# Kernel optimization log

Hardware: AMD Instinct MI355X
Metric: run time of the kernel (lower is better)

The kernel has to match this reference:

```python
import jax, jax.numpy as jnp
from jax import lax
import numpy as np

B, S, D, COMP = 4, 1024, 512, 4


def setup_inputs() -> dict:
    key = jax.random.key(0)
    x = jax.random.normal(key, (B * S, D), dtype=jnp.float32)
    return {"x": x, "comp_rate": COMP, "seqlen": S}


def _merge_step(x, t, seq):
    # x: [seq, D], compacted so the k = seq - t valid tokens occupy rows 0..k-1.
    xn = jnp.roll(x, -1, axis=0)  # x[i+1] (wrap value never selected among valid pairs)
    # dist only feeds argmax (non-differentiable), mirror torch exactly; stop_gradient
    # keeps the vjp from saving residuals for this dead-for-gradients path.
    xg = lax.stop_gradient(x)
    dist = jnp.sum(xg * jnp.roll(xg, -1, axis=0), axis=-1)  # scalar_product metric
    j = jnp.arange(x.shape[0])
    dist = jnp.where(j < seq - 1 - t, dist, -jnp.inf)  # k-1 valid adjacent pairs
    mid = jnp.argmax(dist)
    jm = j[:, None]
    # rows < mid keep, row mid becomes (x[mid]+x[mid+1])/2, rows > mid shift left by 1
    return jnp.where(jm < mid, x, jnp.where(jm == mid, (x + xn) * 0.5, xn))


def _merge_sample(x, steps, seq):
    def body(carry, t):
        return _merge_step(carry, t, seq), None
    x, _ = lax.scan(body, x, jnp.arange(steps))
    return x


def reference(x, comp_rate, seqlen):
    d = x.shape[-1]
    b = x.shape[0] // seqlen
    n_comp = seqlen // comp_rate
    steps = seqlen - n_comp
    xb = x.reshape(b, seqlen, d)
    merged = jax.vmap(lambda xs: _merge_sample(xs, steps, seqlen))(xb)
    # torch smart_merge concatenates per-sample results along dim 0
    return merged[:, :n_comp].reshape(b * n_comp, d)
```

## Files before the change

### kernel.cpp

```cpp
#include <hip/hip_runtime.h>
#include <math.h>

#define S 1024
#define D 512
#define NCOMP (S / 4)
#define STEPS (S - NCOMP)
#define NW 16
#define NEG_INF (-__builtin_inff())

__device__ __forceinline__ int   f2i(float x) { return __builtin_bit_cast(int, x); }
__device__ __forceinline__ float i2f(int x)   { return __builtin_bit_cast(float, x); }

__device__ __forceinline__ unsigned fkey(float f) {
    unsigned u = __builtin_bit_cast(unsigned, f);
    return (u & 0x80000000u) ? ~u : (u | 0x80000000u);
}

__device__ __forceinline__ float wave_sum63(float x) {
    x += i2f(__builtin_amdgcn_update_dpp(0, f2i(x), 0x111, 0xF, 0xF, true));
    x += i2f(__builtin_amdgcn_update_dpp(0, f2i(x), 0x112, 0xF, 0xF, true));
    x += i2f(__builtin_amdgcn_update_dpp(0, f2i(x), 0x114, 0xF, 0xF, true));
    x += i2f(__builtin_amdgcn_update_dpp(0, f2i(x), 0x118, 0xF, 0xF, true));
    x += i2f(__builtin_amdgcn_update_dpp(0, f2i(x), 0x142, 0xA, 0xF, true));
    x += i2f(__builtin_amdgcn_update_dpp(0, f2i(x), 0x143, 0xC, 0xF, true));
    return x;
}

#define AMAX_STEP(ctrl, rm) do {                                                        \
    unsigned ok_ = (unsigned)__builtin_amdgcn_update_dpp((int)key, (int)key, (ctrl), (rm), 0xF, false); \
    int      oi_ = __builtin_amdgcn_update_dpp(bi, bi, (ctrl), (rm), 0xF, false);        \
    bool tk_ = (ok_ > key) || ((ok_ == key) && (oi_ < bi));                              \
    key = tk_ ? ok_ : key; bi = tk_ ? oi_ : bi;                                          \
} while (0)

__device__ __forceinline__ float dot8_partial(float4 a0, float4 a1, float4 b0, float4 b1) {
    float acc = a0.x * b0.x;
    acc += a0.y * b0.y; acc += a0.z * b0.z; acc += a0.w * b0.w;
    acc += a1.x * b1.x; acc += a1.y * b1.y; acc += a1.z * b1.z; acc += a1.w * b1.w;
    return acc;
}

__device__ __forceinline__ void dist_set(float (&dv)[16], bool ln, int k, float val) {
    switch (k) {
        case 0:  if (ln) dv[0]  = val; break;
        case 1:  if (ln) dv[1]  = val; break;
        case 2:  if (ln) dv[2]  = val; break;
        case 3:  if (ln) dv[3]  = val; break;
        case 4:  if (ln) dv[4]  = val; break;
        case 5:  if (ln) dv[5]  = val; break;
        case 6:  if (ln) dv[6]  = val; break;
        case 7:  if (ln) dv[7]  = val; break;
        case 8:  if (ln) dv[8]  = val; break;
        case 9:  if (ln) dv[9]  = val; break;
        case 10: if (ln) dv[10] = val; break;
        case 11: if (ln) dv[11] = val; break;
        case 12: if (ln) dv[12] = val; break;
        case 13: if (ln) dv[13] = val; break;
        case 14: if (ln) dv[14] = val; break;
        case 15: if (ln) dv[15] = val; break;
    }
}

__global__ __launch_bounds__(1024) void pool_merge_kernel(
    const float* __restrict__ x, float* __restrict__ out, float* vals_base) {
    const int b    = blockIdx.x;
    const int tid  = threadIdx.x;
    const int lane = tid & 63;
    const int wave = tid >> 6;

    float* vals = vals_base + (size_t)b * S * D;
    const float* xin = x + (size_t)b * S * D;

    __shared__ int4  links[S];
    __shared__ float sdist[S];
    __shared__ int   outIdx[NCOMP];

    if (vals != (float*)xin) {
        const float4* s4 = (const float4*)xin;
        float4* d4 = (float4*)vals;
        for (int i = tid; i < S * D / 4; i += 1024) d4[i] = s4[i];
    }
    for (int s = tid; s < S; s += 1024)
        links[s] = make_int4(s - 1, s + 1, (s + 2 <= S) ? s + 2 : S, 0);
    __syncthreads();

    for (int pr = wave; pr < S - 1; pr += NW) {
        const float4* a4 = (const float4*)(vals + (size_t)pr * D);
        const float4* b4 = (const float4*)(vals + (size_t)(pr + 1) * D);
        float4 a0 = a4[lane * 2], a1 = a4[lane * 2 + 1];
        float4 b0 = b4[lane * 2], b1 = b4[lane * 2 + 1];
        float tot = wave_sum63(dot8_partial(a0, a1, b0, b1));
        if (lane == 63) sdist[pr] = tot;
    }
    if (tid == 0) sdist[S - 1] = NEG_INF;
    __syncthreads();

    if (wave == 0) {
        float dv[16];
#pragma unroll
        for (int k = 0; k < 16; ++k) dv[k] = sdist[lane + 64 * k];

        for (int t = 0; t < STEPS; ++t) {
            float v8[8]; int k8[8];
#pragma unroll
            for (int k = 0; k < 8; ++k) { bool tk = dv[k+8] > dv[k]; v8[k] = tk ? dv[k+8] : dv[k]; k8[k] = tk ? (k+8) : k; }
            float v4[4]; int k4[4];
#pragma unroll
            for (int k = 0; k < 4; ++k) { bool tk = v8[k+4] > v8[k]; v4[k] = tk ? v8[k+4] : v8[k]; k4[k] = tk ? k8[k+4] : k8[k]; }
            float v2[2]; int k2[2];
#pragma unroll
            for (int k = 0; k < 2; ++k) { bool tk = v4[k+2] > v4[k]; v2[k] = tk ? v4[k+2] : v4[k]; k2[k] = tk ? k4[k+2] : k4[k]; }
            bool tk1 = v2[1] > v2[0];
            float lv = tk1 ? v2[1] : v2[0];
            int   lk = tk1 ? k2[1] : k2[0];

            unsigned key = fkey(lv);
            int bi = lane | (lk << 6);
            AMAX_STEP(0x111, 0xF); AMAX_STEP(0x112, 0xF);
            AMAX_STEP(0x114, 0xF); AMAX_STEP(0x118, 0xF);
            AMAX_STEP(0x142, 0xA); AMAX_STEP(0x143, 0xC);
            const int m = __builtin_amdgcn_readlane(bi, 63);

            int4 L = links[m];
            const int p = __builtin_amdgcn_readfirstlane(L.x);
            const int r = __builtin_amdgcn_readfirstlane(L.y);
            const int q = __builtin_amdgcn_readfirstlane(L.z);
            const bool hasp = (p >= 0), hasq = (q < S);

            const float4* pm = (const float4*)(vals + (size_t)m * D);
            const float4* pr4 = (const float4*)(vals + (size_t)r * D);
            float4 am0 = pm[lane * 2],  am1 = pm[lane * 2 + 1];
            float4 ar0 = pr4[lane * 2], ar1 = pr4[lane * 2 + 1];
            float4 ap0, ap1, aq0, aq1;
            if (hasp) { const float4* pp = (const float4*)(vals + (size_t)p * D); ap0 = pp[lane * 2]; ap1 = pp[lane * 2 + 1]; }
            if (hasq) { const float4* pq = (const float4*)(vals + (size_t)q * D); aq0 = pq[lane * 2]; aq1 = pq[lane * 2 + 1]; }

            int n2r = __builtin_amdgcn_readfirstlane(links[r].z);

            float4 vm0, vm1;
            vm0.x = (am0.x + ar0.x) * 0.5f; vm0.y = (am0.y + ar0.y) * 0.5f;
            vm0.z = (am0.z + ar0.z) * 0.5f; vm0.w = (am0.w + ar0.w) * 0.5f;
            vm1.x = (am1.x + ar1.x) * 0.5f; vm1.y = (am1.y + ar1.y) * 0.5f;
            vm1.z = (am1.z + ar1.z) * 0.5f; vm1.w = (am1.w + ar1.w) * 0.5f;
            ((float4*)(vals + (size_t)m * D))[lane * 2]     = vm0;
            ((float4*)(vals + (size_t)m * D))[lane * 2 + 1] = vm1;

            if (lane == 0) {
                links[m].y = q;
                links[m].z = n2r;
                if (hasp) links[p].z = q;
                if (hasq) links[q].x = m;
            }

            float ndm = NEG_INF, ndp = 0.0f;
            if (hasq) {
                float s_ = wave_sum63(dot8_partial(vm0, vm1, aq0, aq1));
                ndm = i2f(__builtin_amdgcn_readlane(f2i(s_), 63));
            }
            if (hasp) {
                float s_ = wave_sum63(dot8_partial(ap0, ap1, vm0, vm1));
                ndp = i2f(__builtin_amdgcn_readlane(f2i(s_), 63));
            }
            dist_set(dv, lane == (r & 63), r >> 6, NEG_INF);
            dist_set(dv, lane == (m & 63), m >> 6, ndm);
            if (hasp) dist_set(dv, lane == (p & 63), p >> 6, ndp);
        }
    }
    __syncthreads();

    if (tid == 0) {
        int s = 0;
        for (int i = 0; i < NCOMP; ++i) { outIdx[i] = s; s = links[s].y; }
    }
    __syncthreads();

    float* outb = out + (size_t)b * NCOMP * D;
    for (int i = wave; i < NCOMP; i += NW) {
        const float4* sr = (const float4*)(vals + (size_t)outIdx[i] * D);
        float4* dr = (float4*)(outb + (size_t)i * D);
        dr[lane * 2]     = sr[lane * 2];
        dr[lane * 2 + 1] = sr[lane * 2 + 1];
    }
}

extern "C" void kernel_launch(void* const* d_in, const int* in_sizes, int n_in,
                              void* d_out, int out_size, void* d_ws, size_t ws_size,
                              hipStream_t stream) {
    const float* x = (const float*)d_in[0];
    float* out = (float*)d_out;
    const int b = in_sizes[0] / (S * D);
    const size_t need = (size_t)in_sizes[0] * sizeof(float);
    float* vals = (ws_size >= need) ? (float*)d_ws : (float*)x;
    pool_merge_kernel<<<dim3(b), dim3(1024), 0, stream>>>(x, out, vals);
}
```

Before: 1.100 ms.

## Split merge into init/merge/gather kernels with speculative prefetch of next-step rows

Splits the single kernel into three launches. A wide init kernel copies the input and computes the initial adjacent-pair dot products across 16 blocks per sample, a single-wave serial merge kernel runs the loop, and a multi-block gather kernel copies out the kept rows. Inside the merge loop the argmax reads distances from LDS. The rows and links needed for the next step are loaded speculatively for both neighbour-merge cases and for the global-max case, so global-memory latency overlaps the argmax reduction. Intermediate distances and output indices are staged in the output buffer. The trade-offs are extra launches, more complex carry logic and more registers.

Result: faster. 1.052 ms (-4.4%).

```diff
diff --git a/kernel.cpp b/kernel.cpp
--- a/kernel.cpp
+++ b/kernel.cpp
@@ -5,7 +5,6 @@
 #define D 512
 #define NCOMP (S / 4)
 #define STEPS (S - NCOMP)
-#define NW 16
 #define NEG_INF (-__builtin_inff())
 
 __device__ __forceinline__ int   f2i(float x) { return __builtin_bit_cast(int, x); }
@@ -14,6 +13,10 @@
 __device__ __forceinline__ unsigned fkey(float f) {
     unsigned u = __builtin_bit_cast(unsigned, f);
     return (u & 0x80000000u) ? ~u : (u | 0x80000000u);
+}
+__device__ __forceinline__ float unfkey(unsigned k) {
+    unsigned u = (k & 0x80000000u) ? (k & 0x7fffffffu) : ~k;
+    return __builtin_bit_cast(float, u);
 }
 
 __device__ __forceinline__ float wave_sum63(float x) {
@@ -33,153 +36,214 @@
     key = tk_ ? ok_ : key; bi = tk_ ? oi_ : bi;                                          \
 } while (0)
 
-__device__ __forceinline__ float dot8_partial(float4 a0, float4 a1, float4 b0, float4 b1) {
-    float acc = a0.x * b0.x;
-    acc += a0.y * b0.y; acc += a0.z * b0.z; acc += a0.w * b0.w;
-    acc += a1.x * b1.x; acc += a1.y * b1.y; acc += a1.z * b1.z; acc += a1.w * b1.w;
+struct Row { float4 a, b; };
+
+__device__ __forceinline__ Row row_load(const float* vals, int slot, int lane) {
+    const float4* p = (const float4*)(vals + (size_t)slot * D);
+    Row r; r.a = p[lane * 2]; r.b = p[lane * 2 + 1]; return r;
+}
+__device__ __forceinline__ void row_store(float* vals, int slot, int lane, Row r) {
+    float4* p = (float4*)(vals + (size_t)slot * D);
+    p[lane * 2] = r.a; p[lane * 2 + 1] = r.b;
+}
+__device__ __forceinline__ Row row_avg(Row x, Row y) {
+    Row r;
+    r.a.x = (x.a.x + y.a.x) * 0.5f; r.a.y = (x.a.y + y.a.y) * 0.5f;
+    r.a.z = (x.a.z + y.a.z) * 0.5f; r.a.w = (x.a.w + y.a.w) * 0.5f;
+    r.b.x = (x.b.x + y.b.x) * 0.5f; r.b.y = (x.b.y + y.b.y) * 0.5f;
+    r.b.z = (x.b.z + y.b.z) * 0.5f; r.b.w = (x.b.w + y.b.w) * 0.5f;
+    return r;
+}
+__device__ __forceinline__ float dot8_partial(Row x, Row y) {
+    float acc = x.a.x * y.a.x;
+    acc += x.a.y * y.a.y; acc += x.a.z * y.a.z; acc += x.a.w * y.a.w;
+    acc += x.b.x * y.b.x; acc += x.b.y * y.b.y; acc += x.b.z * y.b.z; acc += x.b.w * y.b.w;
     return acc;
 }
-
-__device__ __forceinline__ void dist_set(float (&dv)[16], bool ln, int k, float val) {
-    switch (k) {
-        case 0:  if (ln) dv[0]  = val; break;
-        case 1:  if (ln) dv[1]  = val; break;
-        case 2:  if (ln) dv[2]  = val; break;
-        case 3:  if (ln) dv[3]  = val; break;
-        case 4:  if (ln) dv[4]  = val; break;
-        case 5:  if (ln) dv[5]  = val; break;
-        case 6:  if (ln) dv[6]  = val; break;
-        case 7:  if (ln) dv[7]  = val; break;
-        case 8:  if (ln) dv[8]  = val; break;
-        case 9:  if (ln) dv[9]  = val; break;
-        case 10: if (ln) dv[10] = val; break;
-        case 11: if (ln) dv[11] = val; break;
-        case 12: if (ln) dv[12] = val; break;
-        case 13: if (ln) dv[13] = val; break;
-        case 14: if (ln) dv[14] = val; break;
-        case 15: if (ln) dv[15] = val; break;
-    }
-}
-
-__global__ __launch_bounds__(1024) void pool_merge_kernel(
-    const float* __restrict__ x, float* __restrict__ out, float* vals_base) {
-    const int b    = blockIdx.x;
-    const int tid  = threadIdx.x;
-    const int lane = tid & 63;
-    const int wave = tid >> 6;
-
-    float* vals = vals_base + (size_t)b * S * D;
-    const float* xin = x + (size_t)b * S * D;
-
-    __shared__ int4  links[S];
-    __shared__ float sdist[S];
-    __shared__ int   outIdx[NCOMP];
-
-    if (vals != (float*)xin) {
-        const float4* s4 = (const float4*)xin;
-        float4* d4 = (float4*)vals;
-        for (int i = tid; i < S * D / 4; i += 1024) d4[i] = s4[i];
-    }
-    for (int s = tid; s < S; s += 1024)
-        links[s] = make_int4(s - 1, s + 1, (s + 2 <= S) ? s + 2 : S, 0);
+__device__ __forceinline__ int lsr(int s) { return ((unsigned)s < (unsigned)S) ? s : 0; }
+__device__ __forceinline__ int lsl(int s) { return ((unsigned)s <= (unsigned)S) ? s : 0; }
+
+__device__ __forceinline__ void lds_argmax(const float* dist, int lane, float& v1, int& i1) {
+    float av[16];
+#pragma unroll
+    for (int k = 0; k < 16; ++k) av[k] = dist[lane + 64 * k];
+    float v8[8]; int k8[8];
+#pragma unroll
+    for (int k = 0; k < 8; ++k) { bool tk = av[k+8] > av[k]; v8[k] = tk ? av[k+8] : av[k]; k8[k] = tk ? (k+8) : k; }
+    float v4[4]; int k4[4];
+#pragma unroll
+    for (int k = 0; k < 4; ++k) { bool tk = v8[k+4] > v8[k]; v4[k] = tk ? v8[k+4] : v8[k]; k4[k] = tk ? k8[k+4] : k8[k]; }
+    float v2[2]; int k2[2];
+#pragma unroll
+    for (int k = 0; k < 2; ++k) { bool tk = v4[k+2] > v4[k]; v2[k] = tk ? v4[k+2] : v4[k]; k2[k] = tk ? k4[k+2] : k4[k]; }
+    bool tk1 = v2[1] > v2[0];
+    float lv = tk1 ? v2[1] : v2[0];
+    int   lk = tk1 ? k2[1] : k2[0];
+    unsigned key = fkey(lv);
+    int bi = lane | (lk << 6);
+    AMAX_STEP(0x111, 0xF); AMAX_STEP(0x112, 0xF);
+    AMAX_STEP(0x114, 0xF); AMAX_STEP(0x118, 0xF);
+    AMAX_STEP(0x142, 0xA); AMAX_STEP(0x143, 0xC);
+    i1 = __builtin_amdgcn_readlane(bi, 63);
+    v1 = unfkey((unsigned)__builtin_amdgcn_readlane((int)key, 63));
+}
+
+__global__ __launch_bounds__(256) void init_kernel(const float* __restrict__ x,
+                                                   float* __restrict__ vals,
+                                                   float* __restrict__ out) {
+    const int blk = blockIdx.x, b = blk >> 4, g = blk & 15;
+    const int tid = threadIdx.x, lane = tid & 63, w = tid >> 6;
+    const float* xb = x + (size_t)b * S * D;
+    if (vals != x) {
+        float* vb = vals + (size_t)b * S * D;
+        const float4* s4 = (const float4*)xb;
+        float4* d4 = (float4*)vb;
+        const int base = g * (S * D / 4 / 16);
+        for (int i = tid; i < S * D / 4 / 16; i += 256) d4[base + i] = s4[base + i];
+    }
+    float* sd = out + (size_t)b * NCOMP * D;
+#pragma unroll 1
+    for (int j = 0; j < 16; ++j) {
+        int pr = g * 64 + w * 16 + j;
+        if (pr < S - 1) {
+            Row A = row_load(xb, pr, lane);
+            Row B = row_load(xb, pr + 1, lane);
+            float t = wave_sum63(dot8_partial(A, B));
+            if (lane == 63) sd[pr] = t;
+        }
+    }
+    if (g == 0 && tid == 0) sd[S - 1] = NEG_INF;
+}
+
+__global__ __launch_bounds__(64) void merge_kernel(float* __restrict__ vals,
+                                                   float* __restrict__ out) {
+    const int b = blockIdx.x, lane = threadIdx.x;
+    float* vb = vals + (size_t)b * S * D;
+    float* aux = out + (size_t)b * NCOMP * D;
+    const float* sd = aux;
+    int* outIdx = (int*)(aux + S);
+
+    __shared__ int4  links[S + 1];
+    __shared__ float dist[S];
+
+#pragma unroll
+    for (int k = 0; k < 16; ++k) {
+        int s = lane + 64 * k;
+        links[s] = make_int4(s - 1, s + 1, (s + 2 <= S) ? (s + 2) : S, 0);
+        dist[s] = sd[s];
+    }
+    if (lane == 0) links[S] = make_int4(S, S, S, 0);
+
+    float v1; int i1;
+    lds_argmax(dist, lane, v1, i1);
+    int m = i1;
+    int4 L0 = links[m];
+    int p = __builtin_amdgcn_readfirstlane(L0.x);
+    int r = __builtin_amdgcn_readfirstlane(L0.y);
+    int q = __builtin_amdgcn_readfirstlane(L0.z);
+    bool hasp = (p >= 0), hasq = (q < S);
+    int pp = hasp ? __builtin_amdgcn_readfirstlane(links[p].x) : -1;
+    int nq = hasq ? __builtin_amdgcn_readfirstlane(links[q].y) : S;
+    Row Rp  = row_load(vb, lsr(p),  lane);
+    Row Rm  = row_load(vb, m,       lane);
+    Row Rr  = row_load(vb, r,       lane);
+    Row Rq  = row_load(vb, lsr(q),  lane);
+    Row Rpp = row_load(vb, lsr(pp), lane);
+    Row Rnq = row_load(vb, lsr(nq), lane);
+
+#pragma unroll 1
+    for (int t = 0; t < STEPS; ++t) {
+        if (lane == 0) {
+            links[m].y = q; links[m].z = nq;
+            if (hasp) links[p].z = q;
+            if (hasq) links[q].x = m;
+            dist[m] = NEG_INF; dist[r] = NEG_INF;
+            if (hasp) dist[p] = NEG_INF;
+        }
+        Row vm = row_avg(Rm, Rr);
+        row_store(vb, m, lane, vm);
+        if (t + 1 >= STEPS) break;
+
+        float sp_ = wave_sum63(dot8_partial(Rp, vm));
+        float sq_ = wave_sum63(dot8_partial(vm, Rq));
+        float ndp = hasp ? i2f(__builtin_amdgcn_readlane(f2i(sp_), 63)) : NEG_INF;
+        float ndm = hasq ? i2f(__builtin_amdgcn_readlane(f2i(sq_), 63)) : NEG_INF;
+
+        lds_argmax(dist, lane, v1, i1);
+
+        float best = v1; int bi = i1;
+        if (hasp && (ndp > best || (ndp == best && p < bi))) { best = ndp; bi = p; }
+        if (hasq && (ndm > best || (ndm == best && m < bi))) { best = ndm; bi = m; }
+        const int m2 = bi;
+
+        if (lane == 0) {
+            if (hasp) dist[p] = ndp;
+            if (hasq) dist[m] = ndm;
+        }
+
+        int4 Li = links[lsl(i1)];
+        int p2 = __builtin_amdgcn_readfirstlane(Li.x);
+        int r2 = __builtin_amdgcn_readfirstlane(Li.y);
+        int q2 = __builtin_amdgcn_readfirstlane(Li.z);
+        int4 Lp2 = links[lsl(p2)];
+        int4 Lq2 = links[lsl(q2)];
+        int pp2 = (p2 >= 0) ? __builtin_amdgcn_readfirstlane(Lp2.x) : -1;
+        int nq2 = (q2 < S)  ? __builtin_amdgcn_readfirstlane(Lq2.y) : S;
+        Row Sp  = (p2 == m)  ? vm : row_load(vb, lsr(p2),  lane);
+        Row Si  = row_load(vb, lsr(i1), lane);
+        Row Sr  = row_load(vb, lsr(r2), lane);
+        Row Sq  = (q2 == m)  ? vm : row_load(vb, lsr(q2),  lane);
+        Row Spp = (pp2 == m) ? vm : row_load(vb, lsr(pp2), lane);
+        Row Snq = (nq2 == m) ? vm : row_load(vb, lsr(nq2), lane);
+
+        if (m2 == m) {
+            int nnq = S;
+            if (nq < S) nnq = __builtin_amdgcn_readfirstlane(links[nq].y);
+            Row Rnq2 = (nnq < S) ? row_load(vb, lsr(nnq), lane) : Rnq;
+            Rm = vm; Rr = Rq; Rq = Rnq; Rnq = Rnq2;
+            r = q; q = nq; nq = nnq;
+            hasq = (q < S);
+        } else if (m2 == p) {
+            int npp = -1;
+            if (pp >= 0) npp = __builtin_amdgcn_readfirstlane(links[pp].x);
+            Row Rpp2 = (npp >= 0) ? row_load(vb, lsr(npp), lane) : Rpp;
+            Rr = vm; Rm = Rp; Rp = Rpp; Rpp = Rpp2;
+            r = m; m = p; p = pp; pp = npp;
+            hasp = (p >= 0);
+        } else {
+            m = i1; p = p2; r = r2; q = q2; pp = pp2; nq = nq2;
+            Rm = Si; Rr = Sr; Rp = Sp; Rq = Sq; Rpp = Spp; Rnq = Snq;
+            hasp = (p >= 0); hasq = (q < S);
+        }
+    }
+
+    if (lane == 0) {
+        int s = 0;
+        for (int i = 0; i < NCOMP; i += 2) {
+            outIdx[i] = s;
+            int4 Ls = links[s];
+            if (i + 1 < NCOMP) outIdx[i + 1] = Ls.y;
+            s = Ls.z;
+        }
+    }
+}
+
+__global__ __launch_bounds__(256) void gather_kernel(const float* __restrict__ vals,
+                                                     float* __restrict__ out) {
+    const int b = blockIdx.x, part = blockIdx.y;
+    const float* vb = vals + (size_t)b * S * D;
+    float* ob = out + (size_t)b * NCOMP * D;
+    __shared__ int oi[NCOMP / 8];
+    const int row0 = part * (NCOMP / 8);
+    if (threadIdx.x < NCOMP / 8)
+        oi[threadIdx.x] = ((const int*)(ob + S))[row0 + threadIdx.x];
     __syncthreads();
-
-    for (int pr = wave; pr < S - 1; pr += NW) {
-        const float4* a4 = (const float4*)(vals + (size_t)pr * D);
-        const float4* b4 = (const float4*)(vals + (size_t)(pr + 1) * D);
-        float4 a0 = a4[lane * 2], a1 = a4[lane * 2 + 1];
-        float4 b0 = b4[lane * 2], b1 = b4[lane * 2 + 1];
-        float tot = wave_sum63(dot8_partial(a0, a1, b0, b1));
-        if (lane == 63) sdist[pr] = tot;
-    }
-    if (tid == 0) sdist[S - 1] = NEG_INF;
-    __syncthreads();
-
-    if (wave == 0) {
-        float dv[16];
-#pragma unroll
-        for (int k = 0; k < 16; ++k) dv[k] = sdist[lane + 64 * k];
-
-        for (int t = 0; t < STEPS; ++t) {
-            float v8[8]; int k8[8];
-#pragma unroll
-            for (int k = 0; k < 8; ++k) { bool tk = dv[k+8] > dv[k]; v8[k] = tk ? dv[k+8] : dv[k]; k8[k] = tk ? (k+8) : k; }
-            float v4[4]; int k4[4];
-#pragma unroll
-            for (int k = 0; k < 4; ++k) { bool tk = v8[k+4] > v8[k]; v4[k] = tk ? v8[k+4] : v8[k]; k4[k] = tk ? k8[k+4] : k8[k]; }
-            float v2[2]; int k2[2];
-#pragma unroll
-            for (int k = 0; k < 2; ++k) { bool tk = v4[k+2] > v4[k]; v2[k] = tk ? v4[k+2] : v4[k]; k2[k] = tk ? k4[k+2] : k4[k]; }
-            bool tk1 = v2[1] > v2[0];
-            float lv = tk1 ? v2[1] : v2[0];
-            int   lk = tk1 ? k2[1] : k2[0];
-
-            unsigned key = fkey(lv);
-            int bi = lane | (lk << 6);
-            AMAX_STEP(0x111, 0xF); AMAX_STEP(0x112, 0xF);
-            AMAX_STEP(0x114, 0xF); AMAX_STEP(0x118, 0xF);
-            AMAX_STEP(0x142, 0xA); AMAX_STEP(0x143, 0xC);
-            const int m = __builtin_amdgcn_readlane(bi, 63);
-
-            int4 L = links[m];
-            const int p = __builtin_amdgcn_readfirstlane(L.x);
-            const int r = __builtin_amdgcn_readfirstlane(L.y);
-            const int q = __builtin_amdgcn_readfirstlane(L.z);
-            const bool hasp = (p >= 0), hasq = (q < S);
-
-            const float4* pm = (const float4*)(vals + (size_t)m * D);
-            const float4* pr4 = (const float4*)(vals + (size_t)r * D);
-            float4 am0 = pm[lane * 2],  am1 = pm[lane * 2 + 1];
-            float4 ar0 = pr4[lane * 2], ar1 = pr4[lane * 2 + 1];
-            float4 ap0, ap1, aq0, aq1;
-            if (hasp) { const float4* pp = (const float4*)(vals + (size_t)p * D); ap0 = pp[lane * 2]; ap1 = pp[lane * 2 + 1]; }
-            if (hasq) { const float4* pq = (const float4*)(vals + (size_t)q * D); aq0 = pq[lane * 2]; aq1 = pq[lane * 2 + 1]; }
-
-            int n2r = __builtin_amdgcn_readfirstlane(links[r].z);
-
-            float4 vm0, vm1;
-            vm0.x = (am0.x + ar0.x) * 0.5f; vm0.y = (am0.y + ar0.y) * 0.5f;
-            vm0.z = (am0.z + ar0.z) * 0.5f; vm0.w = (am0.w + ar0.w) * 0.5f;
-            vm1.x = (am1.x + ar1.x) * 0.5f; vm1.y = (am1.y + ar1.y) * 0.5f;
-            vm1.z = (am1.z + ar1.z) * 0.5f; vm1.w = (am1.w + ar1.w) * 0.5f;
-            ((float4*)(vals + (size_t)m * D))[lane * 2]     = vm0;
-            ((float4*)(vals + (size_t)m * D))[lane * 2 + 1] = vm1;
-
-            if (lane == 0) {
-                links[m].y = q;
-                links[m].z = n2r;
-                if (hasp) links[p].z = q;
-                if (hasq) links[q].x = m;
-            }
-
-            float ndm = NEG_INF, ndp = 0.0f;
-            if (hasq) {
-                float s_ = wave_sum63(dot8_partial(vm0, vm1, aq0, aq1));
-                ndm = i2f(__builtin_amdgcn_readlane(f2i(s_), 63));
-            }
-            if (hasp) {
-                float s_ = wave_sum63(dot8_partial(ap0, ap1, vm0, vm1));
-                ndp = i2f(__builtin_amdgcn_readlane(f2i(s_), 63));
-            }
-            dist_set(dv, lane == (r & 63), r >> 6, NEG_INF);
-            dist_set(dv, lane == (m & 63), m >> 6, ndm);
-            if (hasp) dist_set(dv, lane == (p & 63), p >> 6, ndp);
-        }
-    }
-    __syncthreads();
-
-    if (tid == 0) {
-        int s = 0;
-        for (int i = 0; i < NCOMP; ++i) { outIdx[i] = s; s = links[s].y; }
-    }
-    __syncthreads();
-
-    float* outb = out + (size_t)b * NCOMP * D;
-    for (int i = wave; i < NCOMP; i += NW) {
-        const float4* sr = (const float4*)(vals + (size_t)outIdx[i] * D);
-        float4* dr = (float4*)(outb + (size_t)i * D);
-        dr[lane * 2]     = sr[lane * 2];
-        dr[lane * 2 + 1] = sr[lane * 2 + 1];
+    const float4* v4 = (const float4*)vb;
+    float4* o4 = (float4*)ob;
+    const int per = (NCOMP / 8) * (D / 4);
+    for (int idx = threadIdx.x; idx < per; idx += 256) {
+        int row = idx >> 7, c = idx & 127;
+        o4[(size_t)(row0 + row) * (D / 4) + c] = v4[(size_t)oi[row] * (D / 4) + c];
     }
 }
 
@@ -191,5 +255,7 @@
     const int b = in_sizes[0] / (S * D);
     const size_t need = (size_t)in_sizes[0] * sizeof(float);
     float* vals = (ws_size >= need) ? (float*)d_ws : (float*)x;
-    pool_merge_kernel<<<dim3(b), dim3(1024), 0, stream>>>(x, out, vals);
-}
+    init_kernel<<<dim3(16 * b), dim3(256), 0, stream>>>(x, vals, out);
+    merge_kernel<<<dim3(b), dim3(64), 0, stream>>>(vals, out);
+    gather_kernel<<<dim3(b, 8), dim3(256), 0, stream>>>(vals, out);
+}
```
